# Optimization experiments

Measured on AMD Instinct MI355X. Metric: run time of the kernel, lower is better.

## Reference

```python
import jax, jax.numpy as jnp
import numpy as np
from jax import lax

C = 512
B, H, W = 16, 32, 32
PROP_ROUNDS = 5


def _conv(x, w, b, pad):
    # x: [B,Cin,H,W], w: [Cout,Cin,kh,kw]
    y = lax.conv_general_dilated(x, w, (1, 1), [(pad, pad), (pad, pad)],
                                 dimension_numbers=('NCHW', 'OIHW', 'NCHW'))
    return y + b[None, :, None, None]


def _attention(ex, q):
    # torch: A = ex_flat^T @ q_flat ; Bm = softmax(A^T, dim=1) ; att = q_flat @ Bm
    b, c, h, w = q.shape
    ef = ex.reshape(b, c, h * w)   # [B,C,N] exemplar positions n
    qf = q.reshape(b, c, h * w)    # [B,C,M] query positions m
    A = jnp.einsum('bcn,bcm->bnm', ef, qf)   # [B,N,M]
    S = jax.nn.softmax(A, axis=-1)           # softmax over query positions m
    att = jnp.einsum('bcm,bnm->bcn', qf, S)  # [B,C,N]
    return att.reshape(b, c, h, w)


def _gru(x, h, w_r, b_r, w_u, b_u, w_c, b_c):
    # standard ConvGRUCell, kernel_size=1 (padding 0)
    xh = jnp.concatenate([x, h], axis=1)
    r = jax.nn.sigmoid(_conv(xh, w_r, b_r, 0))
    u = jax.nn.sigmoid(_conv(xh, w_u, b_u, 0))
    c = jnp.tanh(_conv(jnp.concatenate([x, r * h], axis=1), w_c, b_c, 0))
    return h * (1.0 - u) + c * u


def setup_inputs() -> dict:
    key = jax.random.key(0)
    ks = jax.random.split(key, 8)
    f = lambda k, s: jax.random.normal(k, s, dtype=jnp.float32)
    return {
        'input1': f(ks[0], (B, C, H, W)),
        'input2': f(ks[1], (B, C, H, W)),
        'input3': f(ks[2], (B, C, H, W)),
        'w_fusion': f(ks[3], (C, 2 * C, 3, 3)) * 0.01,
        'b_fusion': jnp.zeros((C,), jnp.float32),
        'w_out': f(ks[4], (C, 2 * C, 3, 3)) * 0.01,
        'b_out': jnp.zeros((C,), jnp.float32),
        'w_reset': f(ks[5], (C, 2 * C, 1, 1)) * 0.01,
        'b_reset': jnp.zeros((C,), jnp.float32),
        'w_update': f(ks[6], (C, 2 * C, 1, 1)) * 0.01,
        'b_update': jnp.zeros((C,), jnp.float32),
        'w_cand': f(ks[7], (C, 2 * C, 1, 1)) * 0.01,
        'b_cand': jnp.zeros((C,), jnp.float32),
    }


def reference(input1, input2, input3, w_fusion, b_fusion, w_out, b_out,
              w_reset, b_reset, w_update, b_update, w_cand, b_cand):
    # Batched over B (per-item torch loop is mathematically independent per item).
    ex, q, q1 = input1, input2, input3
    gru = lambda x, h: _gru(x, h, w_reset, b_reset, w_update, b_update, w_cand, b_cand)
    for _ in range(PROP_ROUNDS):
        a1 = _conv(jnp.concatenate([_attention(ex, q), _attention(ex, q1)], 1), w_fusion, b_fusion, 1)
        a2 = _conv(jnp.concatenate([_attention(q, ex), _attention(q, q1)], 1), w_fusion, b_fusion, 1)
        a3 = _conv(jnp.concatenate([_attention(q1, ex), _attention(q1, q)], 1), w_fusion, b_fusion, 1)
        ex, q, q1 = gru(a1, ex), gru(a2, q), gru(a3, q1)
    x1 = _conv(jnp.concatenate([ex, input1], 1), w_out, b_out, 1)
    x2 = _conv(jnp.concatenate([q, input2], 1), w_out, b_out, 1)
    x3 = _conv(jnp.concatenate([q1, input3], 1), w_out, b_out, 1)
    return (x1, x2, x3)
```

## Files before the change

### kernel.cpp

```cpp
#include <hip/hip_runtime.h>
#include <hip/hip_bf16.h>


using bf16 = __hip_bfloat16;
typedef __attribute__((ext_vector_type(8))) short bf16x8;
typedef __attribute__((ext_vector_type(4))) float floatx4;

#define MFMA_BF16(a, b, c) __builtin_amdgcn_mfma_f32_16x16x32_bf16((a), (b), (c), 0, 0, 0)

__device__ __forceinline__ void gload_lds16(const bf16* g, bf16* l) {
  __builtin_amdgcn_global_load_lds(
      (__attribute__((address_space(1))) void*)(g),
      (__attribute__((address_space(3))) void*)(l), 16, 0, 0);
}

__device__ __forceinline__ int swz_off(int row, int seg) {
  return row * 32 + ((seg ^ ((row >> 1) & 3)) << 3);
}

__device__ __forceinline__ void stage128x32_async(const bf16* src, int ld,
                                                  bf16* lds, int tid) {
  int r = tid >> 2;
  int seg_log = (((tid & 3) ^ ((tid >> 3) & 3))) * 8;
  gload_lds16(src + (size_t)r * ld + seg_log, lds + tid * 8);
  gload_lds16(src + (size_t)(r + 64) * ld + seg_log, lds + tid * 8 + 2048);
}

__device__ __forceinline__ void mfma_tile(const bf16* la, const bf16* lb,
                                          int wm, int wn, int fm, int fq,
                                          floatx4 (&acc)[4][4]) {
  bf16x8 af[4], bfr[4];
#pragma unroll
  for (int i = 0; i < 4; i++)
    af[i] = *(const bf16x8*)(la + swz_off(wm + i * 16 + fm, fq));
#pragma unroll
  for (int j = 0; j < 4; j++)
    bfr[j] = *(const bf16x8*)(lb + swz_off(wn + j * 16 + fm, fq));
#pragma unroll
  for (int i = 0; i < 4; i++)
#pragma unroll
    for (int j = 0; j < 4; j++)
      acc[i][j] = MFMA_BF16(af[i], bfr[j], acc[i][j]);
}

__device__ __forceinline__ float sigmoidf_(float x) { return 1.0f / (1.0f + __expf(-x)); }
__device__ __forceinline__ unsigned short bfbits(float x) {
  bf16 h = __float2bfloat16(x);
  return *reinterpret_cast<unsigned short*>(&h);
}

__global__ void k_detect(const unsigned short* __restrict__ in, int* __restrict__ flag) {
  if (threadIdx.x == 0 && blockIdx.x == 0) {
    int cnt = 0;
    for (int i = 0; i < 512; i++) {
      int e = (in[i] >> 7) & 0xFF;
      if (e >= 114 && e <= 140) cnt++;
      }
    *flag = (cnt >= 450) ? 1 : 0;
  }
}

__global__ __launch_bounds__(256) void k_cvt(const void* __restrict__ src,
                                             bf16* __restrict__ dst,
                                             const int* __restrict__ flag, int n) {
  int i = blockIdx.x * 256 + threadIdx.x;
  if (i >= n) return;
  if (*flag)
    dst[i] = ((const bf16*)src)[i];
  else
    dst[i] = __float2bfloat16(((const float*)src)[i]);
}

__global__ __launch_bounds__(256, 2) void k_gram(const bf16* __restrict__ X,
                                                 const bf16* __restrict__ Y,
                                                 float* __restrict__ G) {
  int b = blockIdx.z;
  const bf16* Ab = X + (size_t)b * 524288 + (size_t)blockIdx.x * 128 * 512;
  const bf16* Bb = Y + (size_t)b * 524288 + (size_t)blockIdx.y * 128 * 512;
  __shared__ __align__(16) bf16 la[4096], lb[4096];
  int tid = threadIdx.x, wave = tid >> 6, lane = tid & 63;
  int wm = (wave & 1) * 64, wn = (wave >> 1) * 64, fm = lane & 15, fq = lane >> 4;
  floatx4 acc[4][4] = {};
  for (int kc = 0; kc < 512; kc += 32) {
    __syncthreads();
    stage128x32_async(Ab + kc, 512, la, tid);
    stage128x32_async(Bb + kc, 512, lb, tid);
    __syncthreads();
    mfma_tile(la, lb, wm, wn, fm, fq, acc);
  }
  size_t gb = (size_t)b * 1048576;
  int row0 = blockIdx.x * 128 + wm + fq * 4;
  int col0 = blockIdx.y * 128 + wn + fm;
#pragma unroll
  for (int i = 0; i < 4; i++)
#pragma unroll
    for (int j = 0; j < 4; j++)
#pragma unroll
      for (int r = 0; r < 4; r++)
        G[gb + (size_t)(row0 + i * 16 + r) * 1024 + col0 + j * 16] = acc[i][j][r];
}

__global__ __launch_bounds__(256) void k_softmax(float* __restrict__ G) {
  size_t row = blockIdx.x;
  float* g = G + row * 1024;
  int tid = threadIdx.x, wave = tid >> 6, lane = tid & 63;
  float4 x = ((const float4*)g)[tid];
  float m = fmaxf(fmaxf(x.x, x.y), fmaxf(x.z, x.w));
  for (int off = 32; off > 0; off >>= 1) m = fmaxf(m, __shfl_xor(m, off));
  __shared__ float red[4], red2[4];
  if (lane == 0) red[wave] = m;
  __syncthreads();
  m = fmaxf(fmaxf(red[0], red[1]), fmaxf(red[2], red[3]));
  float e0 = __expf(x.x - m), e1 = __expf(x.y - m);
  float e2 = __expf(x.z - m), e3 = __expf(x.w - m);
  float s = e0 + e1 + e2 + e3;
  for (int off = 32; off > 0; off >>= 1) s += __shfl_xor(s, off);
  if (lane == 0) red2[wave] = s;
  __syncthreads();
  float inv = 1.0f / (red2[0] + red2[1] + red2[2] + red2[3]);
  ushort4 o;
  o.x = bfbits(e0 * inv); o.y = bfbits(e1 * inv);
  o.z = bfbits(e2 * inv); o.w = bfbits(e3 * inv);
  ((ushort4*)((bf16*)g))[tid] = o;
}

__global__ __launch_bounds__(256, 2) void k_att(const bf16* __restrict__ S,
                                                const bf16* __restrict__ Ycn,
                                                bf16* __restrict__ out) {
  int b = blockIdx.z;
  const bf16* Ab = S + (size_t)b * 2097152 + (size_t)blockIdx.x * 128 * 2048;
  const bf16* Bb = Ycn + (size_t)b * 524288 + (size_t)blockIdx.y * 128 * 1024;
  __shared__ __align__(16) bf16 la[4096], lb[4096];
  int tid = threadIdx.x, wave = tid >> 6, lane = tid & 63;
  int wm = (wave & 1) * 64, wn = (wave >> 1) * 64, fm = lane & 15, fq = lane >> 4;
  floatx4 acc[4][4] = {};
  for (int kc = 0; kc < 1024; kc += 32) {
    __syncthreads();
    stage128x32_async(Ab + kc, 2048, la, tid);
    stage128x32_async(Bb + kc, 1024, lb, tid);
    __syncthreads();
    mfma_tile(la, lb, wm, wn, fm, fq, acc);
  }
  size_t ob = (size_t)b * 524288;
  int row0 = blockIdx.x * 128 + wm + fq * 4;
  int col0 = blockIdx.y * 128 + wn + fm;
#pragma unroll
  for (int i = 0; i < 4; i++)
#pragma unroll
    for (int j = 0; j < 4; j++)
#pragma unroll
      for (int r = 0; r < 4; r++)
        out[ob + (size_t)(row0 + i * 16 + r) * 512 + col0 + j * 16] =
            __float2bfloat16(acc[i][j][r]);
}

__global__ __launch_bounds__(256, 2) void k_gru01(const bf16* __restrict__ xb,
                                                  const bf16* __restrict__ hb,
                                                  const bf16* __restrict__ wR,
                                                  const bf16* __restrict__ bR,
                                                  const bf16* __restrict__ wU,
                                                  const bf16* __restrict__ bU,
                                                  bf16* __restrict__ rh_out,
                                                  bf16* __restrict__ u_out) {
  size_t row0 = (size_t)blockIdx.x * 128;
  int y = blockIdx.y;
  bool isR = (y < 4);
  int yy = isR ? y : (y - 4);
  const bf16* W = (isR ? wR : wU) + (size_t)yy * 128 * 1024;
  const bf16* bias = isR ? bR : bU;
  bf16* outp = isR ? rh_out : u_out;
  __shared__ __align__(16) bf16 la[4096], lb[4096];
  int tid = threadIdx.x, wave = tid >> 6, lane = tid & 63;
  int wm = (wave & 1) * 64, wn = (wave >> 1) * 64, fm = lane & 15, fq = lane >> 4;
  floatx4 acc[4][4] = {};
  for (int kc = 0; kc < 1024; kc += 32) {
    __syncthreads();
    const bf16* s_ = (kc < 512) ? (xb + row0 * 512 + kc) : (hb + row0 * 512 + (kc - 512));
    stage128x32_async(s_, 512, la, tid);
    stage128x32_async(W + kc, 1024, lb, tid);
    __syncthreads();
    mfma_tile(la, lb, wm, wn, fm, fq, acc);
  }
  int r0 = wm + fq * 4;
  int c0 = yy * 128 + wn + fm;
#pragma unroll
  for (int i = 0; i < 4; i++)
#pragma unroll
    for (int j = 0; j < 4; j++) {
      int co = c0 + j * 16;
      float bj = __bfloat162float(bias[co]);
#pragma unroll
      for (int r = 0; r < 4; r++) {
        size_t idx = (row0 + r0 + i * 16 + r) * 512 + co;
        float v = sigmoidf_(acc[i][j][r] + bj);
        if (isR)
          outp[idx] = __float2bfloat16(v * __bfloat162float(hb[idx]));
        else
          outp[idx] = __float2bfloat16(v);
      }
    }
}

__global__ __launch_bounds__(256, 2) void k_gru2(const bf16* __restrict__ xb,
                                                 const bf16* __restrict__ rhb,
                                                 const bf16* __restrict__ W,
                                                 const bf16* __restrict__ bias,
                                                 bf16* __restrict__ h_state,
                                                 const bf16* __restrict__ u_buf) {
  size_t row0 = (size_t)blockIdx.x * 128;
  const bf16* Wb = W + (size_t)blockIdx.y * 128 * 1024;
  __shared__ __align__(16) bf16 la[4096], lb[4096];
  int tid = threadIdx.x, wave = tid >> 6, lane = tid & 63;
  int wm = (wave & 1) * 64, wn = (wave >> 1) * 64, fm = lane & 15, fq = lane >> 4;
  floatx4 acc[4][4] = {};
  for (int kc = 0; kc < 1024; kc += 32) {
    __syncthreads();
    const bf16* s_ = (kc < 512) ? (xb + row0 * 512 + kc) : (rhb + row0 * 512 + (kc - 512));
    stage128x32_async(s_, 512, la, tid);
    stage128x32_async(Wb + kc, 1024, lb, tid);
    __syncthreads();
    mfma_tile(la, lb, wm, wn, fm, fq, acc);
  }
  int r0 = wm + fq * 4;
  int c0 = blockIdx.y * 128 + wn + fm;
#pragma unroll
  for (int i = 0; i < 4; i++)
#pragma unroll
    for (int j = 0; j < 4; j++) {
      int co = c0 + j * 16;
      float bj = __bfloat162float(bias[co]);
#pragma unroll
      for (int r = 0; r < 4; r++) {
        size_t idx = (row0 + r0 + i * 16 + r) * 512 + co;
        float cv = tanhf(acc[i][j][r] + bj);
        float uu = __bfloat162float(u_buf[idx]);
        float h = __bfloat162float(h_state[idx]);
        h_state[idx] = __float2bfloat16(h * (1.0f - uu) + cv * uu);
      }
    }
}

__global__ __launch_bounds__(256, 3) void k_conv3(const bf16* __restrict__ src0,
                                                  const bf16* __restrict__ src1,
                                                  const bf16* __restrict__ wT,
                                                  const bf16* __restrict__ bias,
                                                  bf16* __restrict__ out) {
  int z = blockIdx.z;
  int y0 = blockIdx.x * 4;
  int co0 = blockIdx.y * 128;
  __shared__ __align__(16) bf16 lin[6528];
  __shared__ __align__(16) bf16 lw[3][4096];
  int tid = threadIdx.x, wave = tid >> 6, lane = tid & 63;
  int wm = (wave & 1) * 64, wn = (wave >> 1) * 64, fm = lane & 15, fq = lane >> 4;
  floatx4 acc[4][4] = {};
  const bf16* s0 = src0 + (size_t)z * 524288;
  const bf16* s1 = src1 + (size_t)z * 524288;
  int r_ = tid >> 2;
  int segl_ = (((tid & 3) ^ ((tid >> 3) & 3))) * 8;

  int sl_p[4], sl_sg[4], sl_off[4];
  bool sl_v[4];
#pragma unroll
  for (int k = 0; k < 4; k++) {
    int slot = k * 256 + tid;
    int sl = slot < 816 ? slot : 815;
    int p = sl >> 2, sg = sl & 3;
    int yy = p / 34, xx = p - yy * 34;
    int y = y0 + yy - 1, x = xx - 1;
    sl_v[k] = (slot < 816) && (y >= 0) && (y <= 31) && (x >= 0) && (x <= 31);
    int yc = min(max(y, 0), 31), xc = min(max(x, 0), 31);
    sl_p[k] = p; sl_sg[k] = sg;
    sl_off[k] = (yc * 32 + xc) * 512 + sg * 8;
  }
  bf16x8 lreg[4];
  const bf16x8 zero8 = {0, 0, 0, 0, 0, 0, 0, 0};

  auto lin_load = [&](int cc) {
    const bf16* sb = (cc < 16) ? (s0 + cc * 32) : (s1 + (cc - 16) * 32);
#pragma unroll
    for (int k = 0; k < 4; k++)
      lreg[k] = *(const bf16x8*)(sb + sl_off[k]);
  };
  auto lin_write = [&]() {
#pragma unroll
    for (int k = 0; k < 4; k++)
      if (k * 256 + tid < 816)
        *(bf16x8*)(lin + swz_off(sl_p[k], sl_sg[k])) = sl_v[k] ? lreg[k] : zero8;
  };
  auto issueW = [&](int cc, int t) {
    const bf16* wsrc = wT + ((size_t)t * 512 + co0) * 1024 + cc * 32;
    bf16* dst = lw[t % 3];
    gload_lds16(wsrc + (size_t)r_ * 1024 + segl_, dst + tid * 8);
    gload_lds16(wsrc + (size_t)(r_ + 64) * 1024 + segl_, dst + tid * 8 + 2048);
  };

  lin_load(0);
  lin_write();
  issueW(0, 0);
  issueW(0, 1);
  asm volatile("s_waitcnt lgkmcnt(0)" ::: "memory");

  for (int cc = 0; cc < 32; cc++) {
#pragma unroll
    for (int t = 0; t < 9; t++) {
      if (t == 1 || t == 2)
        asm volatile("s_waitcnt vmcnt(6)" ::: "memory");
      else
        asm volatile("s_waitcnt vmcnt(2)" ::: "memory");
      if (t == 0)
        asm volatile("s_waitcnt lgkmcnt(0)" ::: "memory");
      __builtin_amdgcn_s_barrier();
      __builtin_amdgcn_sched_barrier(0);
      int dy = t / 3 - 1, dx = t % 3 - 1;
      bf16x8 af[4], bfr[4];
#pragma unroll
      for (int i = 0; i < 4; i++) {
        int j = wm + i * 16 + fm;
        int jy = j >> 5, jx = j & 31;
        int p = (jy + dy + 1) * 34 + (jx + dx + 1);
        af[i] = *(const bf16x8*)(lin + swz_off(p, fq));
      }
#pragma unroll
      for (int jj = 0; jj < 4; jj++)
        bfr[jj] = *(const bf16x8*)(lw[t % 3] + swz_off(wn + jj * 16 + fm, fq));
      {
        int tt = t + 2;
        int ccn = cc + (tt >= 9 ? 1 : 0);
        int tn = tt >= 9 ? tt - 9 : tt;
        if (ccn >= 32) ccn = 0;
        issueW(ccn, tn);
      }
      if (t == 0) {
        __builtin_amdgcn_sched_barrier(0);
        lin_load(cc < 31 ? cc + 1 : cc);
        __builtin_amdgcn_sched_barrier(0);
      }
      asm volatile("s_waitcnt lgkmcnt(0)" ::: "memory");
      __builtin_amdgcn_sched_barrier(0);
      __builtin_amdgcn_s_setprio(1);
#pragma unroll
      for (int i = 0; i < 4; i++)
#pragma unroll
        for (int jj = 0; jj < 4; jj++)
          acc[i][jj] = MFMA_BF16(af[i], bfr[jj], acc[i][jj]);
      __builtin_amdgcn_s_setprio(0);
      __builtin_amdgcn_sched_barrier(0);
    }
    __builtin_amdgcn_s_barrier();
    __builtin_amdgcn_sched_barrier(0);
    lin_write();
  }
  asm volatile("s_waitcnt vmcnt(0)" ::: "memory");

  size_t ob = (size_t)z * 524288;
  int row0 = blockIdx.x * 128 + wm + fq * 4;
  int c0 = co0 + wn + fm;
#pragma unroll
  for (int i = 0; i < 4; i++)
#pragma unroll
    for (int jj = 0; jj < 4; jj++) {
      int co = c0 + jj * 16;
      float bj = __bfloat162float(bias[co]);
#pragma unroll
      for (int r = 0; r < 4; r++)
        out[ob + (size_t)(row0 + i * 16 + r) * 512 + co] =
            __float2bfloat16(acc[i][jj][r] + bj);
    }
}

__global__ __launch_bounds__(256) void k_transpose(const bf16* __restrict__ src,
                                                   bf16* __restrict__ dst,
                                                   int R, int C) {
  __shared__ bf16 t[32][33];
  size_t zoff = (size_t)blockIdx.z * R * C;
  int c0 = blockIdx.x * 32, r0 = blockIdx.y * 32;
  int x = threadIdx.x & 31, y4 = (threadIdx.x >> 5) * 4;
#pragma unroll
  for (int i = 0; i < 4; i++)
    t[y4 + i][x] = src[zoff + (size_t)(r0 + y4 + i) * C + c0 + x];
  __syncthreads();
#pragma unroll
  for (int i = 0; i < 4; i++)
    dst[zoff + (size_t)(c0 + y4 + i) * R + r0 + x] = t[x][y4 + i];
}

__global__ __launch_bounds__(256) void k_store(const bf16* __restrict__ src,
                                               void* __restrict__ dst,
                                               const int* __restrict__ flag) {
  __shared__ bf16 t[32][33];
  size_t zoff = (size_t)blockIdx.z * 524288;
  int c0 = blockIdx.x * 32, r0 = blockIdx.y * 32;
  int x = threadIdx.x & 31, y4 = (threadIdx.x >> 5) * 4;
#pragma unroll
  for (int i = 0; i < 4; i++)
    t[y4 + i][x] = src[zoff + (size_t)(r0 + y4 + i) * 512 + c0 + x];
  __syncthreads();
  bool isbf = (*flag != 0);
#pragma unroll
  for (int i = 0; i < 4; i++) {
    bf16 v = t[x][y4 + i];
    size_t o = zoff + (size_t)(c0 + y4 + i) * 1024 + r0 + x;
    if (isbf) ((bf16*)dst)[o] = v;
    else ((float*)dst)[o] = __bfloat162float(v);
  }
}

__global__ __launch_bounds__(256) void k_init(const void* __restrict__ in1,
                                              const void* __restrict__ in2,
                                              const void* __restrict__ in3,
                                              bf16* __restrict__ state_h,
                                              bf16* __restrict__ state_c,
                                              const int* __restrict__ flag) {
  int z = blockIdx.z, s = z >> 4, b = z & 15;
  const void* srcv = (s == 0 ? in1 : (s == 1 ? in2 : in3));
  bool isbf = (*flag != 0);
  size_t base = (size_t)b * 524288;
  size_t dz = (size_t)z * 524288;
  int n0 = blockIdx.x * 32, c0 = blockIdx.y * 32;
  __shared__ bf16 t[32][33];
  int x = threadIdx.x & 31, y4 = (threadIdx.x >> 5) * 4;
#pragma unroll
  for (int i = 0; i < 4; i++) {
    size_t off = base + (size_t)(c0 + y4 + i) * 1024 + n0 + x;
    bf16 v = isbf ? ((const bf16*)srcv)[off]
                  : __float2bfloat16(((const float*)srcv)[off]);
    t[y4 + i][x] = v;
    state_c[dz + (size_t)(c0 + y4 + i) * 1024 + n0 + x] = v;
  }
  __syncthreads();
#pragma unroll
  for (int i = 0; i < 4; i++)
    state_h[dz + (size_t)(n0 + y4 + i) * 512 + c0 + x] = t[x][y4 + i];
}

__global__ __launch_bounds__(256) void k_in_nhwc(const void* __restrict__ in1,
                                                 const void* __restrict__ in2,
                                                 const void* __restrict__ in3,
                                                 bf16* __restrict__ dst,
                                                 const int* __restrict__ flag) {
  int z = blockIdx.z, s = z >> 4, b = z & 15;
  const void* srcv = (s == 0 ? in1 : (s == 1 ? in2 : in3));
  bool isbf = (*flag != 0);
  size_t base = (size_t)b * 524288;
  size_t dz = (size_t)z * 524288;
  int n0 = blockIdx.x * 32, c0 = blockIdx.y * 32;
  __shared__ bf16 t[32][33];
  int x = threadIdx.x & 31, y4 = (threadIdx.x >> 5) * 4;
#pragma unroll
  for (int i = 0; i < 4; i++) {
    size_t off = base + (size_t)(c0 + y4 + i) * 1024 + n0 + x;
    t[y4 + i][x] = isbf ? ((const bf16*)srcv)[off]
                        : __float2bfloat16(((const float*)srcv)[off]);
  }
  __syncthreads();
#pragma unroll
  for (int i = 0; i < 4; i++)
    dst[dz + (size_t)(n0 + y4 + i) * 512 + c0 + x] = t[x][y4 + i];
}

__global__ __launch_bounds__(256) void k_wtrans(const void* __restrict__ w,
                                                bf16* __restrict__ wT,
                                                const int* __restrict__ flag) {
  int idx = blockIdx.x * 256 + threadIdx.x;
  bool isbf = (*flag != 0);
#pragma unroll
  for (int t = 0; t < 9; t++) {
    bf16 v = isbf ? ((const bf16*)w)[(size_t)idx * 9 + t]
                  : __float2bfloat16(((const float*)w)[(size_t)idx * 9 + t]);
    wT[(size_t)t * 524288 + idx] = v;
  }
}

extern "C" void kernel_launch(void* const* d_in, const int* in_sizes, int n_in,
                              void* d_out, int out_size, void* d_ws, size_t ws_size,
                              hipStream_t stream) {
  (void)in_sizes; (void)n_in; (void)out_size; (void)ws_size;
  const void* in1 = d_in[0];
  const void* in2 = d_in[1];
  const void* in3 = d_in[2];

  char* ws = (char*)d_ws;
  bf16* state_h = (bf16*)(ws + 0);
  bf16* state_c = (bf16*)(ws + 50331648);
  bf16* AttA    = (bf16*)(ws + 100663296);
  bf16* RHbuf   = (bf16*)(ws + 100663296);
  bf16* in_nhwc = (bf16*)(ws + 100663296);
  bf16* AttB    = (bf16*)(ws + 150994944);
  bf16* Ubuf    = (bf16*)(ws + 150994944);
  bf16* OutTmp  = (bf16*)(ws + 150994944);
  float* Gbuf   = (float*)(ws + 201326592);
  bf16* Sbuf    = (bf16*)(ws + 201326592);
  bf16* wT_out  = (bf16*)(ws + 201326592);
  bf16* wT_fus  = (bf16*)(ws + 234881024);
  bf16* wR      = (bf16*)(ws + 244318208);
  bf16* wU      = (bf16*)(ws + 245366784);
  bf16* wC      = (bf16*)(ws + 246415360);
  bf16* bF      = (bf16*)(ws + 247463936);
  bf16* bO      = (bf16*)(ws + 247465984);
  bf16* bR      = (bf16*)(ws + 247468032);
  bf16* bU      = (bf16*)(ws + 247470080);
  bf16* bC      = (bf16*)(ws + 247472128);
  int*  flag    = (int*)(ws + 247474176);
  bf16* Abuf    = (bf16*)d_out;

  const size_t SLICE = 16 * 1024 * 512;
  const size_t CHUNK = 8 * 1024 * 512;

  k_detect<<<1, 64, 0, stream>>>((const unsigned short*)d_in[0], flag);
  k_cvt<<<2048, 256, 0, stream>>>(d_in[7], wR, flag, 524288);
  k_cvt<<<2048, 256, 0, stream>>>(d_in[9], wU, flag, 524288);
  k_cvt<<<2048, 256, 0, stream>>>(d_in[11], wC, flag, 524288);
  k_cvt<<<2, 256, 0, stream>>>(d_in[4], bF, flag, 512);
  k_cvt<<<2, 256, 0, stream>>>(d_in[6], bO, flag, 512);
  k_cvt<<<2, 256, 0, stream>>>(d_in[8], bR, flag, 512);
  k_cvt<<<2, 256, 0, stream>>>(d_in[10], bU, flag, 512);
  k_cvt<<<2, 256, 0, stream>>>(d_in[12], bC, flag, 512);
  k_wtrans<<<2048, 256, 0, stream>>>(d_in[3], wT_fus, flag);
  k_init<<<dim3(32, 16, 48), 256, 0, stream>>>(in1, in2, in3, state_h, state_c, flag);

  const int sx[6] = {0, 0, 1, 1, 2, 2};
  const int sy[6] = {1, 2, 0, 2, 0, 1};
  for (int round = 0; round < 5; ++round) {
    for (int p = 0; p < 3; ++p) {
      for (int h = 0; h < 2; ++h) {
        int i = p * 2 + h;
        bf16* attdst = (h == 0 ? AttA : AttB) + p * SLICE;
        for (int cb = 0; cb < 2; ++cb) {
          size_t co = (size_t)cb * CHUNK;
          k_gram<<<dim3(8, 8, 8), 256, 0, stream>>>(
              state_h + sx[i] * SLICE + co, state_h + sy[i] * SLICE + co, Gbuf);
          k_softmax<<<8192, 256, 0, stream>>>(Gbuf);
          k_att<<<dim3(8, 4, 8), 256, 0, stream>>>(
              Sbuf, state_c + sy[i] * SLICE + co, attdst + co);
        }
      }
    }
    k_conv3<<<dim3(8, 4, 48), 256, 0, stream>>>(AttA, AttB, wT_fus, bF, Abuf);
    k_gru01<<<dim3(384, 8), 256, 0, stream>>>(Abuf, state_h, wR, bR, wU, bU,
                                              RHbuf, Ubuf);
    k_gru2<<<dim3(384, 4), 256, 0, stream>>>(Abuf, RHbuf, wC, bC, state_h, Ubuf);
    k_transpose<<<dim3(16, 32, 48), 256, 0, stream>>>(state_h, state_c, 1024, 512);
  }
  k_wtrans<<<2048, 256, 0, stream>>>(d_in[5], wT_out, flag);
  k_in_nhwc<<<dim3(32, 16, 48), 256, 0, stream>>>(in1, in2, in3, in_nhwc, flag);
  k_conv3<<<dim3(8, 4, 48), 256, 0, stream>>>(state_h, in_nhwc, wT_out, bO, OutTmp);
  k_store<<<dim3(16, 32, 48), 256, 0, stream>>>(OutTmp, d_out, flag);
}
```

Baseline: 7.024 ms.

## Triple-buffer LDS staging with async prefetch in GEMM kernels

Result: slower. 7.231 ms (+3.0%).

```diff
diff --git a/kernel.cpp b/kernel.cpp
--- a/kernel.cpp
+++ b/kernel.cpp
@@ -48,6 +48,24 @@
   bf16 h = __float2bfloat16(x);
   return *reinterpret_cast<unsigned short*>(&h);
 }
+
+#define PIPE_LOOP(NK, STAGE_EXPR, COMPUTE_EXPR)                                \
+  do {                                                                         \
+    { int ks = 0; STAGE_EXPR; }                                                \
+    { int ks = 1; STAGE_EXPR; }                                                \
+    for (int ks_ = 0; ks_ < (NK); ks_++) {                                     \
+      { int ks = ks_ + 2; STAGE_EXPR; }                                        \
+      asm volatile("s_waitcnt vmcnt(8)" ::: "memory");                         \
+      __builtin_amdgcn_s_barrier();                                            \
+      __builtin_amdgcn_sched_barrier(0);                                       \
+      __builtin_amdgcn_s_setprio(1);                                           \
+      { int ks = ks_; COMPUTE_EXPR; }                                          \
+      __builtin_amdgcn_s_setprio(0);                                           \
+      asm volatile("s_waitcnt lgkmcnt(0)" ::: "memory");                       \
+      __builtin_amdgcn_s_barrier();                                            \
+    }                                                                          \
+    asm volatile("s_waitcnt vmcnt(0)" ::: "memory");                           \
+  } while (0)
 
 __global__ void k_detect(const unsigned short* __restrict__ in, int* __restrict__ flag) {
   if (threadIdx.x == 0 && blockIdx.x == 0) {
@@ -77,17 +95,15 @@
   int b = blockIdx.z;
   const bf16* Ab = X + (size_t)b * 524288 + (size_t)blockIdx.x * 128 * 512;
   const bf16* Bb = Y + (size_t)b * 524288 + (size_t)blockIdx.y * 128 * 512;
-  __shared__ __align__(16) bf16 la[4096], lb[4096];
+  __shared__ __align__(16) bf16 la[3][4096], lb[3][4096];
   int tid = threadIdx.x, wave = tid >> 6, lane = tid & 63;
   int wm = (wave & 1) * 64, wn = (wave >> 1) * 64, fm = lane & 15, fq = lane >> 4;
   floatx4 acc[4][4] = {};
-  for (int kc = 0; kc < 512; kc += 32) {
-    __syncthreads();
-    stage128x32_async(Ab + kc, 512, la, tid);
-    stage128x32_async(Bb + kc, 512, lb, tid);
-    __syncthreads();
-    mfma_tile(la, lb, wm, wn, fm, fq, acc);
-  }
+  PIPE_LOOP(16,
+    { int kk = (ks < 16 ? ks : 0) * 32; int bu = ks % 3;
+      stage128x32_async(Ab + kk, 512, la[bu], tid);
+      stage128x32_async(Bb + kk, 512, lb[bu], tid); },
+    { mfma_tile(la[ks % 3], lb[ks % 3], wm, wn, fm, fq, acc); });
   size_t gb = (size_t)b * 1048576;
   int row0 = blockIdx.x * 128 + wm + fq * 4;
   int col0 = blockIdx.y * 128 + wn + fm;
@@ -130,17 +146,15 @@
   int b = blockIdx.z;
   const bf16* Ab = S + (size_t)b * 2097152 + (size_t)blockIdx.x * 128 * 2048;
   const bf16* Bb = Ycn + (size_t)b * 524288 + (size_t)blockIdx.y * 128 * 1024;
-  __shared__ __align__(16) bf16 la[4096], lb[4096];
+  __shared__ __align__(16) bf16 la[3][4096], lb[3][4096];
   int tid = threadIdx.x, wave = tid >> 6, lane = tid & 63;
   int wm = (wave & 1) * 64, wn = (wave >> 1) * 64, fm = lane & 15, fq = lane >> 4;
   floatx4 acc[4][4] = {};
-  for (int kc = 0; kc < 1024; kc += 32) {
-    __syncthreads();
-    stage128x32_async(Ab + kc, 2048, la, tid);
-    stage128x32_async(Bb + kc, 1024, lb, tid);
-    __syncthreads();
-    mfma_tile(la, lb, wm, wn, fm, fq, acc);
-  }
+  PIPE_LOOP(32,
+    { int kk = (ks < 32 ? ks : 0) * 32; int bu = ks % 3;
+      stage128x32_async(Ab + kk, 2048, la[bu], tid);
+      stage128x32_async(Bb + kk, 1024, lb[bu], tid); },
+    { mfma_tile(la[ks % 3], lb[ks % 3], wm, wn, fm, fq, acc); });
   size_t ob = (size_t)b * 524288;
   int row0 = blockIdx.x * 128 + wm + fq * 4;
   int col0 = blockIdx.y * 128 + wn + fm;
@@ -169,18 +183,17 @@
   const bf16* W = (isR ? wR : wU) + (size_t)yy * 128 * 1024;
   const bf16* bias = isR ? bR : bU;
   bf16* outp = isR ? rh_out : u_out;
-  __shared__ __align__(16) bf16 la[4096], lb[4096];
+  __shared__ __align__(16) bf16 la[3][4096], lb[3][4096];
   int tid = threadIdx.x, wave = tid >> 6, lane = tid & 63;
   int wm = (wave & 1) * 64, wn = (wave >> 1) * 64, fm = lane & 15, fq = lane >> 4;
   floatx4 acc[4][4] = {};
-  for (int kc = 0; kc < 1024; kc += 32) {
-    __syncthreads();
-    const bf16* s_ = (kc < 512) ? (xb + row0 * 512 + kc) : (hb + row0 * 512 + (kc - 512));
-    stage128x32_async(s_, 512, la, tid);
-    stage128x32_async(W + kc, 1024, lb, tid);
-    __syncthreads();
-    mfma_tile(la, lb, wm, wn, fm, fq, acc);
-  }
+  PIPE_LOOP(32,
+    { int kc = (ks < 32 ? ks : 0) * 32; int bu = ks % 3;
+      const bf16* s_ = (kc < 512) ? (xb + row0 * 512 + kc)
+                                  : (hb + row0 * 512 + (kc - 512));
+      stage128x32_async(s_, 512, la[bu], tid);
+      stage128x32_async(W + kc, 1024, lb[bu], tid); },
+    { mfma_tile(la[ks % 3], lb[ks % 3], wm, wn, fm, fq, acc); });
   int r0 = wm + fq * 4;
   int c0 = yy * 128 + wn + fm;
 #pragma unroll
@@ -209,18 +222,17 @@
                                                  const bf16* __restrict__ u_buf) {
   size_t row0 = (size_t)blockIdx.x * 128;
   const bf16* Wb = W + (size_t)blockIdx.y * 128 * 1024;
-  __shared__ __align__(16) bf16 la[4096], lb[4096];
+  __shared__ __align__(16) bf16 la[3][4096], lb[3][4096];
   int tid = threadIdx.x, wave = tid >> 6, lane = tid & 63;
   int wm = (wave & 1) * 64, wn = (wave >> 1) * 64, fm = lane & 15, fq = lane >> 4;
   floatx4 acc[4][4] = {};
-  for (int kc = 0; kc < 1024; kc += 32) {
-    __syncthreads();
-    const bf16* s_ = (kc < 512) ? (xb + row0 * 512 + kc) : (rhb + row0 * 512 + (kc - 512));
-    stage128x32_async(s_, 512, la, tid);
-    stage128x32_async(Wb + kc, 1024, lb, tid);
-    __syncthreads();
-    mfma_tile(la, lb, wm, wn, fm, fq, acc);
-  }
+  PIPE_LOOP(32,
+    { int kc = (ks < 32 ? ks : 0) * 32; int bu = ks % 3;
+      const bf16* s_ = (kc < 512) ? (xb + row0 * 512 + kc)
+                                  : (rhb + row0 * 512 + (kc - 512));
+      stage128x32_async(s_, 512, la[bu], tid);
+      stage128x32_async(Wb + kc, 1024, lb[bu], tid); },
+    { mfma_tile(la[ks % 3], lb[ks % 3], wm, wn, fm, fq, acc); });
   int r0 = wm + fq * 4;
   int c0 = blockIdx.y * 128 + wn + fm;
 #pragma unroll
```

## Fuse softmax into attention GEMM, computing row stats and exponentials on the fly

Applied to the files above, without the earlier changes.

Result: slower. 7.993 ms (+13.8%).

```diff
diff --git a/kernel.cpp b/kernel.cpp
--- a/kernel.cpp
+++ b/kernel.cpp
@@ -100,57 +100,89 @@
         G[gb + (size_t)(row0 + i * 16 + r) * 1024 + col0 + j * 16] = acc[i][j][r];
 }
 
-__global__ __launch_bounds__(256) void k_softmax(float* __restrict__ G) {
-  size_t row = blockIdx.x;
-  float* g = G + row * 1024;
+__global__ __launch_bounds__(256, 2) void k_att3(const float* __restrict__ G,
+                                                 const bf16* __restrict__ Ycn,
+                                                 bf16* __restrict__ out) {
+  int bid = blockIdx.x;
+  int x2 = ((bid & 7) << 2) | (bid >> 3);
+  int z = blockIdx.y;
+  const float* Gb = G + (size_t)z * 1048576 + (size_t)x2 * 32 * 1024;
+  const bf16* Yb = Ycn + (size_t)z * 524288;
+  __shared__ __align__(16) bf16 la[1024];
+  __shared__ __align__(16) bf16 lb[16384];
+  __shared__ float sstat[64];
   int tid = threadIdx.x, wave = tid >> 6, lane = tid & 63;
-  float4 x = ((const float4*)g)[tid];
-  float m = fmaxf(fmaxf(x.x, x.y), fmaxf(x.z, x.w));
-  for (int off = 32; off > 0; off >>= 1) m = fmaxf(m, __shfl_xor(m, off));
-  __shared__ float red[4], red2[4];
-  if (lane == 0) red[wave] = m;
+  int fm = lane & 15, fq = lane >> 4;
+
+  for (int rr = 0; rr < 8; rr++) {
+    int row = wave * 8 + rr;
+    const float4* g4 = (const float4*)(Gb + (size_t)row * 1024);
+    float4 v0 = g4[lane], v1 = g4[lane + 64];
+    float4 v2 = g4[lane + 128], v3 = g4[lane + 192];
+    float m = fmaxf(fmaxf(fmaxf(fmaxf(v0.x, v0.y), fmaxf(v0.z, v0.w)),
+                          fmaxf(fmaxf(v1.x, v1.y), fmaxf(v1.z, v1.w))),
+                    fmaxf(fmaxf(fmaxf(v2.x, v2.y), fmaxf(v2.z, v2.w)),
+                          fmaxf(fmaxf(v3.x, v3.y), fmaxf(v3.z, v3.w))));
+    for (int off = 32; off > 0; off >>= 1) m = fmaxf(m, __shfl_xor(m, off));
+    float s = __expf(v0.x - m) + __expf(v0.y - m) + __expf(v0.z - m) + __expf(v0.w - m)
+            + __expf(v1.x - m) + __expf(v1.y - m) + __expf(v1.z - m) + __expf(v1.w - m)
+            + __expf(v2.x - m) + __expf(v2.y - m) + __expf(v2.z - m) + __expf(v2.w - m)
+            + __expf(v3.x - m) + __expf(v3.y - m) + __expf(v3.z - m) + __expf(v3.w - m);
+    for (int off = 32; off > 0; off >>= 1) s += __shfl_xor(s, off);
+    if (lane == 0) { sstat[row] = m; sstat[32 + row] = 1.0f / s; }
+  }
   __syncthreads();
-  m = fmaxf(fmaxf(red[0], red[1]), fmaxf(red[2], red[3]));
-  float e0 = __expf(x.x - m), e1 = __expf(x.y - m);
-  float e2 = __expf(x.z - m), e3 = __expf(x.w - m);
-  float s = e0 + e1 + e2 + e3;
-  for (int off = 32; off > 0; off >>= 1) s += __shfl_xor(s, off);
-  if (lane == 0) red2[wave] = s;
-  __syncthreads();
-  float inv = 1.0f / (red2[0] + red2[1] + red2[2] + red2[3]);
-  ushort4 o;
-  o.x = bfbits(e0 * inv); o.y = bfbits(e1 * inv);
-  o.z = bfbits(e2 * inv); o.w = bfbits(e3 * inv);
-  ((ushort4*)((bf16*)g))[tid] = o;
-}
-
-__global__ __launch_bounds__(256, 2) void k_att(const bf16* __restrict__ S,
-                                                const bf16* __restrict__ Ycn,
-                                                bf16* __restrict__ out) {
-  int b = blockIdx.z;
-  const bf16* Ab = S + (size_t)b * 2097152 + (size_t)blockIdx.x * 128 * 2048;
-  const bf16* Bb = Ycn + (size_t)b * 524288 + (size_t)blockIdx.y * 128 * 1024;
-  __shared__ __align__(16) bf16 la[4096], lb[4096];
-  int tid = threadIdx.x, wave = tid >> 6, lane = tid & 63;
-  int wm = (wave & 1) * 64, wn = (wave >> 1) * 64, fm = lane & 15, fq = lane >> 4;
-  floatx4 acc[4][4] = {};
+
+  bool doLa = (tid < 128);
+  int lrow = tid >> 2, lsg = tid & 3;
+  float sm = 0.0f, sinv = 0.0f;
+  if (doLa) { sm = sstat[lrow]; sinv = sstat[32 + lrow]; }
+
+  floatx4 acc[2][8] = {};
   for (int kc = 0; kc < 1024; kc += 32) {
     __syncthreads();
-    stage128x32_async(Ab + kc, 2048, la, tid);
-    stage128x32_async(Bb + kc, 1024, lb, tid);
-    __syncthreads();
-    mfma_tile(la, lb, wm, wn, fm, fq, acc);
-  }
-  size_t ob = (size_t)b * 524288;
-  int row0 = blockIdx.x * 128 + wm + fq * 4;
-  int col0 = blockIdx.y * 128 + wn + fm;
-#pragma unroll
-  for (int i = 0; i < 4; i++)
-#pragma unroll
-    for (int j = 0; j < 4; j++)
+    stage128x32_async(Yb + kc, 1024, lb, tid);
+    stage128x32_async(Yb + 131072 + kc, 1024, lb + 4096, tid);
+    stage128x32_async(Yb + 262144 + kc, 1024, lb + 8192, tid);
+    stage128x32_async(Yb + 393216 + kc, 1024, lb + 12288, tid);
+    if (doLa) {
+      const float* gs = Gb + (size_t)lrow * 1024 + kc + lsg * 8;
+      float4 a = *(const float4*)gs;
+      float4 b4 = *(const float4*)(gs + 4);
+      bf16x8 p;
+      p[0] = (short)bfbits(__expf(a.x - sm) * sinv);
+      p[1] = (short)bfbits(__expf(a.y - sm) * sinv);
+      p[2] = (short)bfbits(__expf(a.z - sm) * sinv);
+      p[3] = (short)bfbits(__expf(a.w - sm) * sinv);
+      p[4] = (short)bfbits(__expf(b4.x - sm) * sinv);
+      p[5] = (short)bfbits(__expf(b4.y - sm) * sinv);
+      p[6] = (short)bfbits(__expf(b4.z - sm) * sinv);
+      p[7] = (short)bfbits(__expf(b4.w - sm) * sinv);
+      *(bf16x8*)(la + swz_off(lrow, lsg)) = p;
+    }
+    __syncthreads();
+    bf16x8 af[2], bfr[8];
+    af[0] = *(const bf16x8*)(la + swz_off(fm, fq));
+    af[1] = *(const bf16x8*)(la + swz_off(16 + fm, fq));
+#pragma unroll
+    for (int j = 0; j < 8; j++)
+      bfr[j] = *(const bf16x8*)(lb + swz_off(wave * 128 + j * 16 + fm, fq));
+#pragma unroll
+    for (int i = 0; i < 2; i++)
+#pragma unroll
+      for (int j = 0; j < 8; j++)
+        acc[i][j] = MFMA_BF16(af[i], bfr[j], acc[i][j]);
+  }
+  size_t ob = (size_t)z * 524288;
+  int row0 = x2 * 32 + fq * 4;
+  int c0 = wave * 128 + fm;
+#pragma unroll
+  for (int i = 0; i < 2; i++)
+#pragma unroll
+    for (int j = 0; j < 8; j++)
 #pragma unroll
       for (int r = 0; r < 4; r++)
-        out[ob + (size_t)(row0 + i * 16 + r) * 512 + col0 + j * 16] =
+        out[ob + (size_t)(row0 + i * 16 + r) * 512 + c0 + j * 16] =
             __float2bfloat16(acc[i][j][r]);
 }
 
@@ -489,7 +521,6 @@
   bf16* Ubuf    = (bf16*)(ws + 150994944);
   bf16* OutTmp  = (bf16*)(ws + 150994944);
   float* Gbuf   = (float*)(ws + 201326592);
-  bf16* Sbuf    = (bf16*)(ws + 201326592);
   bf16* wT_out  = (bf16*)(ws + 201326592);
   bf16* wT_fus  = (bf16*)(ws + 234881024);
   bf16* wR      = (bf16*)(ws + 244318208);
@@ -529,9 +560,8 @@
           size_t co = (size_t)cb * CHUNK;
           k_gram<<<dim3(8, 8, 8), 256, 0, stream>>>(
               state_h + sx[i] * SLICE + co, state_h + sy[i] * SLICE + co, Gbuf);
-          k_softmax<<<8192, 256, 0, stream>>>(Gbuf);
-          k_att<<<dim3(8, 4, 8), 256, 0, stream>>>(
-              Sbuf, state_c + sy[i] * SLICE + co, attdst + co);
+          k_att3<<<dim3(32, 8), 256, 0, stream>>>(
+              Gbuf, state_c + sy[i] * SLICE + co, attdst + co);
         }
       }
     }
```
